# Kernel optimization log

Hardware: AMD Instinct MI355X
Metric: run time of the kernel (lower is better)

The kernel has to match this reference:

```python
import jax, jax.numpy as jnp
import numpy as np
from jax import lax

FILTERS = [(1, 32), (2, 32), (3, 64), (4, 128), (5, 256), (6, 512), (7, 1024)]
CHAR_VOCAB, CHAR_DIM, MAX_CHARS = 262, 16, 50
N_FILTERS = sum(n for _, n in FILTERS)  # 2048
PROJ_DIM = 512
B, S = 16, 256


def setup_inputs() -> dict:
    key = jax.random.key(0)
    ks = jax.random.split(key, 32)
    inp = {}
    inp["words"] = jax.random.randint(ks[0], (B, S), 0, 50000)
    inp["chars"] = jax.random.randint(ks[1], (B, S, MAX_CHARS), 0, CHAR_VOCAB)
    inp["char_emb"] = jax.random.normal(ks[2], (CHAR_VOCAB, CHAR_DIM), jnp.float32) * 0.1
    for i, (w, n) in enumerate(FILTERS):
        inp[f"conv_w_{i}"] = jax.random.normal(ks[3 + i], (n, CHAR_DIM, w), jnp.float32) * 0.1
        inp[f"conv_b_{i}"] = jnp.zeros((n,), jnp.float32)
    for j in range(2):
        inp[f"hw_w_{j}"] = jax.random.normal(ks[12 + j], (2 * N_FILTERS, N_FILTERS), jnp.float32) * 0.02
        # Highway init: transform bias = 0, gate bias = 1
        inp[f"hw_b_{j}"] = jnp.concatenate([jnp.zeros((N_FILTERS,), jnp.float32), jnp.ones((N_FILTERS,), jnp.float32)])
    inp["proj_w"] = jax.random.normal(ks[20], (PROJ_DIM, N_FILTERS), jnp.float32) * 0.02
    inp["proj_b"] = jnp.zeros((PROJ_DIM,), jnp.float32)
    return inp


def _char_cnn(chars, char_emb, conv_ws, conv_bs, hw_ws, hw_bs, proj_w, proj_b):
    b, s, L = chars.shape
    # (B*S, CHAR_DIM, L)
    x = char_emb[chars].reshape(b * s, L, -1).transpose(0, 2, 1)
    convs = []
    for w, bias in zip(conv_ws, conv_bs):
        # Conv1d valid, NCW layout; y: (N, num, L-width+1)
        y = lax.conv_general_dilated(x, w, (1,), "VALID", dimension_numbers=("NCH", "OIH", "NCH"))
        y = y + bias[None, :, None]
        y = jnp.max(y, axis=-1)          # max over time
        convs.append(jax.nn.relu(y))      # activation
    h = jnp.concatenate(convs, axis=-1)   # (N, 2048)
    d = h.shape[-1]
    for W, bb in zip(hw_ws, hw_bs):
        p = h @ W.T + bb
        nonlinear = jax.nn.relu(p[:, :d])
        gate = jax.nn.sigmoid(p[:, d:])
        h = gate * h + (1.0 - gate) * nonlinear
    out = h @ proj_w.T + proj_b
    return out.reshape(b, s, -1)


def reference(words, chars, char_emb,
              conv_w_0, conv_b_0, conv_w_1, conv_b_1, conv_w_2, conv_b_2,
              conv_w_3, conv_b_3, conv_w_4, conv_b_4, conv_w_5, conv_b_5,
              conv_w_6, conv_b_6, hw_w_0, hw_b_0, hw_w_1, hw_b_1, proj_w, proj_b):
    conv_ws = [conv_w_0, conv_w_1, conv_w_2, conv_w_3, conv_w_4, conv_w_5, conv_w_6]
    conv_bs = [conv_b_0, conv_b_1, conv_b_2, conv_b_3, conv_b_4, conv_b_5, conv_b_6]
    return _char_cnn(chars, char_emb, conv_ws, conv_bs, [hw_w_0, hw_w_1], [hw_b_0, hw_b_1], proj_w, proj_b)
```

## Files before the change

### kernel.cpp

```cpp
#include <hip/hip_runtime.h>
#include <hip/hip_bf16.h>


#define NTOK 4096
#define NF   2048
#define KDIM 2048
#define HID  4096
#define PDIM 512

typedef __attribute__((ext_vector_type(4))) float floatx4;
typedef __attribute__((ext_vector_type(8))) short shortx8;

__device__ inline void async_copy16(const void* g, void* l) {
  __builtin_amdgcn_global_load_lds(
      (const __attribute__((address_space(1))) void*)(uintptr_t)g,
      (__attribute__((address_space(3))) void*)(uint32_t)(uintptr_t)l,
      16, 0, 0);
}

__global__ __launch_bounds__(256) void cvt_kernel(
    const float* __restrict__ s, __hip_bfloat16* __restrict__ d, int n) {
  int i = blockIdx.x * 256 + threadIdx.x;
  if (i < n) d[i] = __float2bfloat16(s[i]);
}

__global__ __launch_bounds__(256) void cvt_hw(
    const float* __restrict__ s, __hip_bfloat16* __restrict__ d) {
  int i = blockIdx.x * 256 + threadIdx.x;
  int r = i >> 11, k = i & 2047;
  int sr = (r >> 1) + (r & 1) * 2048;
  d[i] = __float2bfloat16(s[(size_t)sr * 2048 + k]);
}

__global__ __launch_bounds__(256) void conv_wprep(
    const float* __restrict__ w0, const float* __restrict__ w1,
    const float* __restrict__ w2, const float* __restrict__ w3,
    const float* __restrict__ w4, const float* __restrict__ w5,
    const float* __restrict__ w6,
    const float* __restrict__ b0, const float* __restrict__ b1,
    const float* __restrict__ b2, const float* __restrict__ b3,
    const float* __restrict__ b4, const float* __restrict__ b5,
    const float* __restrict__ b6, const float* __restrict__ emb,
    __hip_bfloat16* __restrict__ Wb, float* __restrict__ Bc,
    __hip_bfloat16* __restrict__ embb) {
  int idx = blockIdx.x * 256 + threadIdx.x;
  const int start[7] = {0, 32, 64, 128, 256, 512, 1024};
  const float* ws[7] = {w0, w1, w2, w3, w4, w5, w6};
  const float* bs[7] = {b0, b1, b2, b3, b4, b5, b6};
  if (idx < 262144) {
    int ch = idx >> 7, kp = idx & 127;
    int f = (ch >= 32) + (ch >= 64) + (ch >= 128) + (ch >= 256) +
            (ch >= 512) + (ch >= 1024);
    int w = f + 1, lc = ch - start[f];
    int d = kp & 15, k = kp >> 4;
    float v = (k < w) ? ws[f][((size_t)lc * 16 + d) * w + k] : 0.f;
    Wb[idx] = __float2bfloat16(v);
  } else if (idx < 262144 + 2048) {
    int ch = idx - 262144;
    int f = (ch >= 32) + (ch >= 64) + (ch >= 128) + (ch >= 256) +
            (ch >= 512) + (ch >= 1024);
    Bc[ch] = bs[f][ch - start[f]];
  } else if (idx < 262144 + 2048 + 4192) {
    int e = idx - 262144 - 2048;
    embb[e] = __float2bfloat16(emb[e]);
  }
}

template <int NKT, int NT, int ROWS>
__global__ __launch_bounds__(256) void conv_k(
    const int* __restrict__ chars, const __hip_bfloat16* __restrict__ embb,
    const __hip_bfloat16* __restrict__ Wb, const float* __restrict__ bias,
    __hip_bfloat16* __restrict__ h, int chbase) {
  __shared__ __align__(16) __hip_bfloat16 Xs[2 * 4 * ROWS * 24];
  int tid = threadIdx.x, wave = tid >> 6, lane = tid & 63;
  int frow = lane & 15, q = lane >> 4;
  int chb = chbase + blockIdx.y * 64;
  int tokbase = blockIdx.x * 32;

  shortx8 wreg[NKT][4];
#pragma unroll
  for (int kt = 0; kt < NKT; ++kt)
#pragma unroll
    for (int j = 0; j < 4; ++j)
      wreg[kt][j] = *(const shortx8*)(
          Wb + (size_t)(chb + j * 16 + frow) * 128 + kt * 32 + q * 8);

  float blane = bias[chb + lane];
  int Tvj[4];
#pragma unroll
  for (int j = 0; j < 4; ++j) {
    int ch = chb + j * 16 + frow;
    int w = 1 + (ch >= 32) + (ch >= 64) + (ch >= 128) + (ch >= 256) +
            (ch >= 512) + (ch >= 1024);
    Tvj[j] = 51 - w;
  }

  auto stage = [&](int g, int buf) {
    constexpr int NST = 4 * ROWS;
#pragma unroll
    for (int rep = 0; rep < (NST + 255) / 256; ++rep) {
      int rr = tid + rep * 256;
      if (rr < NST) {
        int tk = rr / ROWS, r = rr - tk * ROWS;
        __hip_bfloat16* dst = Xs + ((size_t)(buf * 4 + tk) * ROWS + r) * 24;
        if (r < 50) {
          int c = chars[(size_t)(tokbase + g * 4 + tk) * 50 + r];
          const shortx8* e = (const shortx8*)(embb + c * 16);
          *(shortx8*)(dst) = e[0];
          *(shortx8*)(dst + 8) = e[1];
        } else if (g <= 1) {
          shortx8 z = {0, 0, 0, 0, 0, 0, 0, 0};
          *(shortx8*)(dst) = z;
          *(shortx8*)(dst + 8) = z;
        }
      }
    }
  };

  stage(0, 0);
  __syncthreads();

  const floatx4 zero = {0.f, 0.f, 0.f, 0.f};
#pragma unroll 1
  for (int g = 0; g < 8; ++g) {
    if (g < 7) stage(g + 1, (g + 1) & 1);

    const __hip_bfloat16* Xw = Xs + (size_t)((g & 1) * 4 + wave) * ROWS * 24;
    floatx4 acc[NT][4];

#pragma unroll
    for (int kt = 0; kt < NKT; ++kt) {
      int kk = kt * 2 + (q >> 1);
      int d0 = (q & 1) * 8;
      shortx8 xf[NT];
#pragma unroll
      for (int i = 0; i < NT; ++i)
        xf[i] = *(const shortx8*)(Xw + (i * 16 + frow + kk) * 24 + d0);
#pragma unroll
      for (int i = 0; i < NT; ++i)
#pragma unroll
        for (int j = 0; j < 4; ++j) {
          if (kt == 0)
            acc[i][j] = __builtin_amdgcn_mfma_f32_16x16x32_bf16(
                xf[i], wreg[0][j], zero, 0, 0, 0);
          else
            acc[i][j] = __builtin_amdgcn_mfma_f32_16x16x32_bf16(
                xf[i], wreg[kt][j], acc[i][j], 0, 0, 0);
        }
    }

    float vj[4];
#pragma unroll
    for (int j = 0; j < 4; ++j) {
      float v = -1e30f;
#pragma unroll
      for (int i = 0; i < NT; ++i) {
#pragma unroll
        for (int r = 0; r < 4; ++r) {
          if (i < 2) {
            v = fmaxf(v, acc[i][j][r]);
          } else {
            int t = i * 16 + q * 4 + r;
            if (t < Tvj[j]) v = fmaxf(v, acc[i][j][r]);
          }
        }
      }
      v = fmaxf(v, __shfl_xor(v, 16));
      v = fmaxf(v, __shfl_xor(v, 32));
      vj[j] = v;
    }
    float r0 = (q & 2) ? vj[2] : vj[0];
    float r1 = (q & 2) ? vj[3] : vj[1];
    float rv = (q & 1) ? r1 : r0;
    int tok = tokbase + g * 4 + wave;
    h[(size_t)tok * NF + chb + lane] =
        __float2bfloat16(fmaxf(rv + blane, 0.f));
    __syncthreads();
  }
}

__global__ __launch_bounds__(256) void gemm_hw(
    const __hip_bfloat16* __restrict__ A, const __hip_bfloat16* __restrict__ B,
    const float* __restrict__ hwb, __hip_bfloat16* __restrict__ Hdst) {
  const int K = KDIM;
  __shared__ __align__(16) __hip_bfloat16 As[128 * 64];
  __shared__ __align__(16) __hip_bfloat16 Bs[128 * 64];
  int tid = threadIdx.x;
  int wave = tid >> 6, lane = tid & 63;
  int wr = wave >> 1, wc = wave & 1;
  int bn = blockIdx.y, bm = blockIdx.x;

  int sr8 = lane >> 3;
  int sc8 = lane & 7;
  int frow = lane & 15;
  int q    = lane >> 4;

  floatx4 acc[4][4];
  floatx4 zero = {0.f, 0.f, 0.f, 0.f};
#pragma unroll
  for (int i = 0; i < 4; ++i)
#pragma unroll
    for (int j = 0; j < 4; ++j) acc[i][j] = zero;

  const __hip_bfloat16* Ab = A + (size_t)bn * 128 * K;
  const __hip_bfloat16* Bb = B + (size_t)bm * 128 * K;

  for (int kb = 0; kb < K; kb += 64) {
    __syncthreads();
#pragma unroll
    for (int it = 0; it < 4; ++it) {
      int seg = wave * 4 + it;
      int r = seg * 8 + sr8;
      int gc = sc8 ^ (r & 7);
      async_copy16(Ab + (size_t)r * K + kb + gc * 8, (char*)As + seg * 1024);
      async_copy16(Bb + (size_t)r * K + kb + gc * 8, (char*)Bs + seg * 1024);
    }
    __syncthreads();

#pragma unroll
    for (int s = 0; s < 2; ++s) {
      shortx8 af[4], bf[4];
#pragma unroll
      for (int i = 0; i < 4; ++i) {
        int r = wr * 64 + i * 16 + frow;
        af[i] = *(const shortx8*)(As + r * 64 + ((s * 4 + q) ^ (r & 7)) * 8);
      }
#pragma unroll
      for (int j = 0; j < 4; ++j) {
        int r = wc * 64 + j * 16 + frow;
        bf[j] = *(const shortx8*)(Bs + r * 64 + ((s * 4 + q) ^ (r & 7)) * 8);
      }
#pragma unroll
      for (int i = 0; i < 4; ++i)
#pragma unroll
        for (int j = 0; j < 4; ++j)
          acc[i][j] = __builtin_amdgcn_mfma_f32_16x16x32_bf16(
              af[i], bf[j], acc[i][j], 0, 0, 0);
    }
  }

  int crow0 = bn * 128 + wr * 64 + q * 4;
  int ccol0 = bm * 128 + wc * 64 + frow;
#pragma unroll
  for (int i = 0; i < 4; ++i)
#pragma unroll
    for (int j = 0; j < 4; ++j) {
      int gcol = ccol0 + j * 16;
      float bb = (gcol & 1) ? hwb[2048 + (gcol >> 1)] : hwb[gcol >> 1];
#pragma unroll
      for (int r = 0; r < 4; ++r) {
        int row = crow0 + i * 16 + r;
        float v = acc[i][j][r] + bb;
        float partner = __shfl_xor(v, 1);
        if (!(lane & 1)) {
          float gte = 1.f / (1.f + expf(-partner));
          int ch = gcol >> 1;
          float hold = __bfloat162float(A[(size_t)row * 2048 + ch]);
          float hnew = gte * hold + (1.f - gte) * fmaxf(v, 0.f);
          Hdst[(size_t)row * 2048 + ch] = __float2bfloat16(hnew);
        }
      }
    }
}

__global__ __launch_bounds__(256) void gemm_proj(
    const __hip_bfloat16* __restrict__ A, const __hip_bfloat16* __restrict__ B,
    float* __restrict__ C, const float* __restrict__ bias) {
  const int K = KDIM;
  __shared__ __align__(16) __hip_bfloat16 As[32 * 64];
  __shared__ __align__(16) __hip_bfloat16 Bs[128 * 64];
  int tid = threadIdx.x;
  int wave = tid >> 6, lane = tid & 63;
  int wr = wave >> 1, wc = wave & 1;
  int bn = blockIdx.y, bm = blockIdx.x;

  int sr8 = lane >> 3, sc8 = lane & 7;
  int frow = lane & 15, q = lane >> 4;

  floatx4 acc[4];
  floatx4 zero = {0.f, 0.f, 0.f, 0.f};
#pragma unroll
  for (int j = 0; j < 4; ++j) acc[j] = zero;

  const __hip_bfloat16* Ab = A + (size_t)bn * 32 * K;
  const __hip_bfloat16* Bb = B + (size_t)bm * 128 * K;

  for (int kb = 0; kb < K; kb += 64) {
    __syncthreads();
    {
      int r = wave * 8 + sr8;
      int gc = sc8 ^ (r & 7);
      async_copy16(Ab + (size_t)r * K + kb + gc * 8, (char*)As + wave * 1024);
    }
#pragma unroll
    for (int it = 0; it < 4; ++it) {
      int seg = wave * 4 + it;
      int r = seg * 8 + sr8;
      int gc = sc8 ^ (r & 7);
      async_copy16(Bb + (size_t)r * K + kb + gc * 8, (char*)Bs + seg * 1024);
    }
    __syncthreads();

#pragma unroll
    for (int s = 0; s < 2; ++s) {
      shortx8 af, bf[4];
      {
        int r = wr * 16 + frow;
        af = *(const shortx8*)(As + r * 64 + ((s * 4 + q) ^ (r & 7)) * 8);
      }
#pragma unroll
      for (int j = 0; j < 4; ++j) {
        int r = wc * 64 + j * 16 + frow;
        bf[j] = *(const shortx8*)(Bs + r * 64 + ((s * 4 + q) ^ (r & 7)) * 8);
      }
#pragma unroll
      for (int j = 0; j < 4; ++j)
        acc[j] = __builtin_amdgcn_mfma_f32_16x16x32_bf16(af, bf[j], acc[j],
                                                          0, 0, 0);
    }
  }

  int crow0 = bn * 32 + wr * 16 + q * 4;
  int ccol0 = bm * 128 + wc * 64 + frow;
#pragma unroll
  for (int j = 0; j < 4; ++j) {
    int c = ccol0 + j * 16;
#pragma unroll
    for (int r = 0; r < 4; ++r) {
      int row = crow0 + r;
      C[(size_t)row * PDIM + c] = acc[j][r] + bias[c];
    }
  }
}

extern "C" void kernel_launch(void* const* d_in, const int* in_sizes, int n_in,
                              void* d_out, int out_size, void* d_ws, size_t ws_size,
                              hipStream_t stream) {
  const int*   chars  = (const int*)d_in[1];
  const float* emb    = (const float*)d_in[2];
  const float* cw[7];
  const float* cb[7];
  for (int i = 0; i < 7; ++i) {
    cw[i] = (const float*)d_in[3 + 2 * i];
    cb[i] = (const float*)d_in[4 + 2 * i];
  }
  const float* hw_w0  = (const float*)d_in[17];
  const float* hw_b0  = (const float*)d_in[18];
  const float* hw_w1  = (const float*)d_in[19];
  const float* hw_b1  = (const float*)d_in[20];
  const float* proj_w = (const float*)d_in[21];
  const float* proj_b = (const float*)d_in[22];
  float* out = (float*)d_out;

  char* ws = (char*)d_ws;
  __hip_bfloat16* h      = (__hip_bfloat16*)(ws);
  __hip_bfloat16* h2     = (__hip_bfloat16*)(ws + (16ull << 20));
  __hip_bfloat16* convWb = (__hip_bfloat16*)(ws + (32ull << 20));
  float*          convBc = (float*)(ws + (32ull << 20) + 524288);
  __hip_bfloat16* embb   = (__hip_bfloat16*)(ws + (32ull << 20) + 524288 + 8192);
  __hip_bfloat16* w0b    = (__hip_bfloat16*)(ws + (48ull << 20));
  __hip_bfloat16* w1b    = (__hip_bfloat16*)(ws + (64ull << 20));
  __hip_bfloat16* pwb    = (__hip_bfloat16*)(ws + (80ull << 20));

  cvt_hw<<<(HID * KDIM) / 256, 256, 0, stream>>>(hw_w0, w0b);
  cvt_hw<<<(HID * KDIM) / 256, 256, 0, stream>>>(hw_w1, w1b);
  cvt_kernel<<<(PDIM * KDIM) / 256, 256, 0, stream>>>(proj_w, pwb, PDIM * KDIM);
  conv_wprep<<<(262144 + 2048 + 4192 + 255) / 256, 256, 0, stream>>>(
      cw[0], cw[1], cw[2], cw[3], cw[4], cw[5], cw[6],
      cb[0], cb[1], cb[2], cb[3], cb[4], cb[5], cb[6], emb,
      convWb, convBc, embb);

  conv_k<1, 4, 72><<<dim3(128, 1), 256, 0, stream>>>(chars, embb, convWb,
                                                     convBc, h, 0);
  conv_k<2, 3, 56><<<dim3(128, 3), 256, 0, stream>>>(chars, embb, convWb,
                                                     convBc, h, 64);
  conv_k<3, 3, 56><<<dim3(128, 12), 256, 0, stream>>>(chars, embb, convWb,
                                                      convBc, h, 256);
  conv_k<4, 3, 56><<<dim3(128, 16), 256, 0, stream>>>(chars, embb, convWb,
                                                      convBc, h, 1024);

  gemm_hw<<<dim3(HID / 128, NTOK / 128), 256, 0, stream>>>(h, w0b, hw_b0, h2);
  gemm_hw<<<dim3(HID / 128, NTOK / 128), 256, 0, stream>>>(h2, w1b, hw_b1, h);
  gemm_proj<<<dim3(PDIM / 128, NTOK / 32), 256, 0, stream>>>(h, pwb, out,
                                                             proj_b);
}
```

Before: 520.4 us.

## Merge prep kernels, halve GEMM K-tile, and remap highway block order

Folds the four weight-conversion kernels into one prep_all launch to cut launch overhead. In both GEMMs the K-tile per iteration drops from 64 to 32 and the XOR-swizzled LDS layout is replaced with a plain row layout, which halves shared memory use but doubles the number of barriers per K and may add LDS bank conflicts. The highway GEMM also remaps block ids so groups of 4 row-tiles share column tiles, aiming for better L2 reuse.

```diff
diff --git a/kernel.cpp b/kernel.cpp
--- a/kernel.cpp
+++ b/kernel.cpp
@@ -18,21 +18,17 @@
       16, 0, 0);
 }
 
-__global__ __launch_bounds__(256) void cvt_kernel(
-    const float* __restrict__ s, __hip_bfloat16* __restrict__ d, int n) {
-  int i = blockIdx.x * 256 + threadIdx.x;
-  if (i < n) d[i] = __float2bfloat16(s[i]);
-}
-
-__global__ __launch_bounds__(256) void cvt_hw(
-    const float* __restrict__ s, __hip_bfloat16* __restrict__ d) {
-  int i = blockIdx.x * 256 + threadIdx.x;
-  int r = i >> 11, k = i & 2047;
-  int sr = (r >> 1) + (r & 1) * 2048;
-  d[i] = __float2bfloat16(s[(size_t)sr * 2048 + k]);
-}
-
-__global__ __launch_bounds__(256) void conv_wprep(
+#define PR_W0  0
+#define PR_W1  8388608
+#define PR_PW  16777216
+#define PR_CW  17825792
+#define PR_CB  18087936
+#define PR_EM  18089984
+#define PR_END 18094176
+
+__global__ __launch_bounds__(256) void prep_all(
+    const float* __restrict__ hw_w0, const float* __restrict__ hw_w1,
+    const float* __restrict__ proj_w,
     const float* __restrict__ w0, const float* __restrict__ w1,
     const float* __restrict__ w2, const float* __restrict__ w3,
     const float* __restrict__ w4, const float* __restrict__ w5,
@@ -41,27 +37,40 @@
     const float* __restrict__ b2, const float* __restrict__ b3,
     const float* __restrict__ b4, const float* __restrict__ b5,
     const float* __restrict__ b6, const float* __restrict__ emb,
-    __hip_bfloat16* __restrict__ Wb, float* __restrict__ Bc,
-    __hip_bfloat16* __restrict__ embb) {
+    __hip_bfloat16* __restrict__ w0b, __hip_bfloat16* __restrict__ w1b,
+    __hip_bfloat16* __restrict__ pwb, __hip_bfloat16* __restrict__ Wb,
+    float* __restrict__ Bc, __hip_bfloat16* __restrict__ embb) {
   int idx = blockIdx.x * 256 + threadIdx.x;
+  if (idx >= PR_END) return;
   const int start[7] = {0, 32, 64, 128, 256, 512, 1024};
   const float* ws[7] = {w0, w1, w2, w3, w4, w5, w6};
   const float* bs[7] = {b0, b1, b2, b3, b4, b5, b6};
-  if (idx < 262144) {
-    int ch = idx >> 7, kp = idx & 127;
+  if (idx < PR_PW) {
+    const float* s = (idx < PR_W1) ? hw_w0 : hw_w1;
+    __hip_bfloat16* d = (idx < PR_W1) ? w0b : w1b;
+    int i = (idx < PR_W1) ? idx : idx - PR_W1;
+    int r = i >> 11, k = i & 2047;
+    int sr = (r >> 1) + (r & 1) * 2048;
+    d[i] = __float2bfloat16(s[(size_t)sr * 2048 + k]);
+  } else if (idx < PR_CW) {
+    int i = idx - PR_PW;
+    pwb[i] = __float2bfloat16(proj_w[i]);
+  } else if (idx < PR_CB) {
+    int i = idx - PR_CW;
+    int ch = i >> 7, kp = i & 127;
     int f = (ch >= 32) + (ch >= 64) + (ch >= 128) + (ch >= 256) +
             (ch >= 512) + (ch >= 1024);
     int w = f + 1, lc = ch - start[f];
     int d = kp & 15, k = kp >> 4;
     float v = (k < w) ? ws[f][((size_t)lc * 16 + d) * w + k] : 0.f;
-    Wb[idx] = __float2bfloat16(v);
-  } else if (idx < 262144 + 2048) {
-    int ch = idx - 262144;
+    Wb[i] = __float2bfloat16(v);
+  } else if (idx < PR_EM) {
+    int ch = idx - PR_CB;
     int f = (ch >= 32) + (ch >= 64) + (ch >= 128) + (ch >= 256) +
             (ch >= 512) + (ch >= 1024);
     Bc[ch] = bs[f][ch - start[f]];
-  } else if (idx < 262144 + 2048 + 4192) {
-    int e = idx - 262144 - 2048;
+  } else {
+    int e = idx - PR_EM;
     embb[e] = __float2bfloat16(emb[e]);
   }
 }
@@ -183,16 +192,19 @@
     const __hip_bfloat16* __restrict__ A, const __hip_bfloat16* __restrict__ B,
     const float* __restrict__ hwb, __hip_bfloat16* __restrict__ Hdst) {
   const int K = KDIM;
-  __shared__ __align__(16) __hip_bfloat16 As[128 * 64];
-  __shared__ __align__(16) __hip_bfloat16 Bs[128 * 64];
+  __shared__ __align__(16) __hip_bfloat16 As[128 * 32];
+  __shared__ __align__(16) __hip_bfloat16 Bs[128 * 32];
   int tid = threadIdx.x;
   int wave = tid >> 6, lane = tid & 63;
   int wr = wave >> 1, wc = wave & 1;
-  int bn = blockIdx.y, bm = blockIdx.x;
-
-  int sr8 = lane >> 3;
-  int sc8 = lane & 7;
+  int id = blockIdx.y * 32 + blockIdx.x;
+  int bn = (id >> 7) * 4 + (id & 3);
+  int bm = (id >> 2) & 31;
+
+  int srow = lane >> 2;
+  int skq  = (lane & 3) * 8;
   int frow = lane & 15;
+  int fkq  = (lane >> 4) * 8;
   int q    = lane >> 4;
 
   floatx4 acc[4][4];
@@ -205,38 +217,31 @@
   const __hip_bfloat16* Ab = A + (size_t)bn * 128 * K;
   const __hip_bfloat16* Bb = B + (size_t)bm * 128 * K;
 
-  for (int kb = 0; kb < K; kb += 64) {
-    __syncthreads();
-#pragma unroll
-    for (int it = 0; it < 4; ++it) {
-      int seg = wave * 4 + it;
-      int r = seg * 8 + sr8;
-      int gc = sc8 ^ (r & 7);
-      async_copy16(Ab + (size_t)r * K + kb + gc * 8, (char*)As + seg * 1024);
-      async_copy16(Bb + (size_t)r * K + kb + gc * 8, (char*)Bs + seg * 1024);
-    }
-    __syncthreads();
-
-#pragma unroll
-    for (int s = 0; s < 2; ++s) {
-      shortx8 af[4], bf[4];
-#pragma unroll
-      for (int i = 0; i < 4; ++i) {
-        int r = wr * 64 + i * 16 + frow;
-        af[i] = *(const shortx8*)(As + r * 64 + ((s * 4 + q) ^ (r & 7)) * 8);
-      }
-#pragma unroll
-      for (int j = 0; j < 4; ++j) {
-        int r = wc * 64 + j * 16 + frow;
-        bf[j] = *(const shortx8*)(Bs + r * 64 + ((s * 4 + q) ^ (r & 7)) * 8);
-      }
-#pragma unroll
-      for (int i = 0; i < 4; ++i)
-#pragma unroll
-        for (int j = 0; j < 4; ++j)
-          acc[i][j] = __builtin_amdgcn_mfma_f32_16x16x32_bf16(
-              af[i], bf[j], acc[i][j], 0, 0, 0);
-    }
+  for (int kb = 0; kb < K; kb += 32) {
+    __syncthreads();
+#pragma unroll
+    for (int it = 0; it < 2; ++it) {
+      int seg = wave * 2 + it;
+      async_copy16(Ab + (size_t)(seg * 16 + srow) * K + kb + skq,
+                   (char*)As + seg * 1024);
+      async_copy16(Bb + (size_t)(seg * 16 + srow) * K + kb + skq,
+                   (char*)Bs + seg * 1024);
+    }
+    __syncthreads();
+
+    shortx8 af[4], bf[4];
+#pragma unroll
+    for (int i = 0; i < 4; ++i)
+      af[i] = *(const shortx8*)(As + (wr * 64 + i * 16 + frow) * 32 + fkq);
+#pragma unroll
+    for (int j = 0; j < 4; ++j)
+      bf[j] = *(const shortx8*)(Bs + (wc * 64 + j * 16 + frow) * 32 + fkq);
+#pragma unroll
+    for (int i = 0; i < 4; ++i)
+#pragma unroll
+      for (int j = 0; j < 4; ++j)
+        acc[i][j] =
+            __builtin_amdgcn_mfma_f32_16x16x32_bf16(af[i], bf[j], acc[i][j], 0, 0, 0);
   }
 
   int crow0 = bn * 128 + wr * 64 + q * 4;
@@ -267,15 +272,18 @@
     const __hip_bfloat16* __restrict__ A, const __hip_bfloat16* __restrict__ B,
     float* __restrict__ C, const float* __restrict__ bias) {
   const int K = KDIM;
-  __shared__ __align__(16) __hip_bfloat16 As[32 * 64];
-  __shared__ __align__(16) __hip_bfloat16 Bs[128 * 64];
+  __shared__ __align__(16) __hip_bfloat16 As[32 * 32];
+  __shared__ __align__(16) __hip_bfloat16 Bs[128 * 32];
   int tid = threadIdx.x;
   int wave = tid >> 6, lane = tid & 63;
   int wr = wave >> 1, wc = wave & 1;
   int bn = blockIdx.y, bm = blockIdx.x;
 
-  int sr8 = lane >> 3, sc8 = lane & 7;
-  int frow = lane & 15, q = lane >> 4;
+  int srow = lane >> 2;
+  int skq  = (lane & 3) * 8;
+  int frow = lane & 15;
+  int fkq  = (lane >> 4) * 8;
+  int q    = lane >> 4;
 
   floatx4 acc[4];
   floatx4 zero = {0.f, 0.f, 0.f, 0.f};
@@ -285,39 +293,28 @@
   const __hip_bfloat16* Ab = A + (size_t)bn * 32 * K;
   const __hip_bfloat16* Bb = B + (size_t)bm * 128 * K;
 
-  for (int kb = 0; kb < K; kb += 64) {
-    __syncthreads();
-    {
-      int r = wave * 8 + sr8;
-      int gc = sc8 ^ (r & 7);
-      async_copy16(Ab + (size_t)r * K + kb + gc * 8, (char*)As + wave * 1024);
-    }
-#pragma unroll
-    for (int it = 0; it < 4; ++it) {
-      int seg = wave * 4 + it;
-      int r = seg * 8 + sr8;
-      int gc = sc8 ^ (r & 7);
-      async_copy16(Bb + (size_t)r * K + kb + gc * 8, (char*)Bs + seg * 1024);
-    }
-    __syncthreads();
-
-#pragma unroll
-    for (int s = 0; s < 2; ++s) {
-      shortx8 af, bf[4];
-      {
-        int r = wr * 16 + frow;
-        af = *(const shortx8*)(As + r * 64 + ((s * 4 + q) ^ (r & 7)) * 8);
-      }
-#pragma unroll
-      for (int j = 0; j < 4; ++j) {
-        int r = wc * 64 + j * 16 + frow;
-        bf[j] = *(const shortx8*)(Bs + r * 64 + ((s * 4 + q) ^ (r & 7)) * 8);
-      }
-#pragma unroll
-      for (int j = 0; j < 4; ++j)
-        acc[j] = __builtin_amdgcn_mfma_f32_16x16x32_bf16(af, bf[j], acc[j],
-                                                          0, 0, 0);
-    }
+  for (int kb = 0; kb < K; kb += 32) {
+    __syncthreads();
+    if (wave < 2)
+      async_copy16(Ab + (size_t)(wave * 16 + srow) * K + kb + skq,
+                   (char*)As + wave * 1024);
+#pragma unroll
+    for (int it = 0; it < 2; ++it) {
+      int seg = wave * 2 + it;
+      async_copy16(Bb + (size_t)(seg * 16 + srow) * K + kb + skq,
+                   (char*)Bs + seg * 1024);
+    }
+    __syncthreads();
+
+    shortx8 af, bf[4];
+    af = *(const shortx8*)(As + (wr * 16 + frow) * 32 + fkq);
+#pragma unroll
+    for (int j = 0; j < 4; ++j)
+      bf[j] = *(const shortx8*)(Bs + (wc * 64 + j * 16 + frow) * 32 + fkq);
+#pragma unroll
+    for (int j = 0; j < 4; ++j)
+      acc[j] = __builtin_amdgcn_mfma_f32_16x16x32_bf16(af, bf[j], acc[j],
+                                                        0, 0, 0);
   }
 
   int crow0 = bn * 32 + wr * 16 + q * 4;
@@ -362,13 +359,11 @@
   __hip_bfloat16* w1b    = (__hip_bfloat16*)(ws + (64ull << 20));
   __hip_bfloat16* pwb    = (__hip_bfloat16*)(ws + (80ull << 20));
 
-  cvt_hw<<<(HID * KDIM) / 256, 256, 0, stream>>>(hw_w0, w0b);
-  cvt_hw<<<(HID * KDIM) / 256, 256, 0, stream>>>(hw_w1, w1b);
-  cvt_kernel<<<(PDIM * KDIM) / 256, 256, 0, stream>>>(proj_w, pwb, PDIM * KDIM);
-  conv_wprep<<<(262144 + 2048 + 4192 + 255) / 256, 256, 0, stream>>>(
+  prep_all<<<(PR_END + 255) / 256, 256, 0, stream>>>(
+      hw_w0, hw_w1, proj_w,
       cw[0], cw[1], cw[2], cw[3], cw[4], cw[5], cw[6],
       cb[0], cb[1], cb[2], cb[3], cb[4], cb[5], cb[6], emb,
-      convWb, convBc, embb);
+      w0b, w1b, pwb, convWb, convBc, embb);
 
   conv_k<1, 4, 72><<<dim3(128, 1), 256, 0, stream>>>(chars, embb, convWb,
                                                      convBc, h, 0);
@@ -379,8 +374,8 @@
   conv_k<4, 3, 56><<<dim3(128, 16), 256, 0, stream>>>(chars, embb, convWb,
                                                       convBc, h, 1024);
 
-  gemm_hw<<<dim3(HID / 128, NTOK / 128), 256, 0, stream>>>(h, w0b, hw_b0, h2);
-  gemm_hw<<<dim3(HID / 128, NTOK / 128), 256, 0, stream>>>(h2, w1b, hw_b1, h);
+  gemm_hw<<<dim3(32, 32), 256, 0, stream>>>(h, w0b, hw_b0, h2);
+  gemm_hw<<<dim3(32, 32), 256, 0, stream>>>(h2, w1b, hw_b1, h);
   gemm_proj<<<dim3(PDIM / 128, NTOK / 32), 256, 0, stream>>>(h, pwb, out,
                                                              proj_b);
 }
```

Result: slower. 543.8 us (+4.5%).
